# Optimization experiments

Hardware: AMD Instinct MI355X
Metric: run time of the kernel (lower is better)

The kernel has to match this reference:

```python
import jax, jax.numpy as jnp
import numpy as np

VOCAB = 100000
PAD_ID = 0
INTEREST_ID = 1
B, S, D = 16, 200, 128

def setup_inputs() -> dict:
    key = jax.random.key(0)
    ks = jax.random.split(key, 10)
    sc = 0.05
    return {
        "x": jax.random.normal(ks[0], (B, S, D), jnp.float32),
        "x_ids": jax.random.randint(ks[1], (B, S), 0, VOCAB),
        "Wq": jax.random.normal(ks[2], (D, D), jnp.float32) * sc,
        "bq": jax.random.normal(ks[3], (D,), jnp.float32) * sc,
        "Wk": jax.random.normal(ks[4], (D, D), jnp.float32) * sc,
        "bk": jax.random.normal(ks[5], (D,), jnp.float32) * sc,
        "Wv": jax.random.normal(ks[6], (D, 1), jnp.float32) * sc,
        "bv": jax.random.normal(ks[7], (1,), jnp.float32) * sc,
        "Wec": jax.random.normal(ks[8], (2 * D, VOCAB), jnp.float32) * sc,
        "bec": jax.random.normal(ks[9], (VOCAB,), jnp.float32) * sc,
    }

def reference(x, x_ids, Wq, bq, Wk, bk, Wv, bv, Wec, bec):
    # mask: valid (non-pad, non-interest) positions  (B,S)
    mask = (x_ids != PAD_ID) & (x_ids != INTEREST_ID)
    # additive attention pooling (explore_proj=True)
    q = jnp.einsum('bsd,de->bse', x, Wq) + bq            # (B,S,D)
    k = jnp.einsum('bd,de->be', x[:, 0, :], Wk) + bk      # (B,D), broadcast over S
    features = jnp.tanh(q + k[:, None, :])                # (B,S,D)
    scores = jnp.einsum('bsd,do->bso', features, Wv)[..., 0] + bv[0]  # (B,S)
    scores = jax.nn.softmax(scores, axis=-1)
    c_s = jnp.einsum('bsd,bs->bd', x, scores)             # (B,D)
    h_t = x[:, 0, :]                                      # (B,D)
    c_s = jnp.concatenate([h_t, c_s], axis=-1)            # (B,2D)
    p_explore = c_s @ Wec + bec                           # (B,V)
    # explore_mask: histogram of masked ids over vocab.
    # Equivalent to bmm(mask, one_hot(x_ids)) but O(B*S) scatter instead of O(B*S*V).
    explore_mask = jnp.zeros((x.shape[0], VOCAB), jnp.float32)
    batch_idx = jnp.arange(x.shape[0])[:, None]           # (B,1)
    explore_mask = explore_mask.at[batch_idx, x_ids].add(mask.astype(jnp.float32))
    p_explore = jnp.where(explore_mask > 0, -jnp.inf, p_explore)
    return jax.nn.softmax(p_explore, axis=-1)
```

## Files before the change

### kernel.cpp

```cpp
#include <hip/hip_runtime.h>
#include <cstdint>
#include <cstddef>
#include <math.h>

#define B 16
#define S 200
#define D 128
#define VOCAB 100000
#define V4 (VOCAB / 4)
#define SCH 8
#define VTILE 256
#define NVT ((VOCAB + VTILE - 1) / VTILE)

__global__ __launch_bounds__(128) void k_scores(
    const float* __restrict__ x,
    const float* __restrict__ Wq, const float* __restrict__ bq,
    const float* __restrict__ Wk, const float* __restrict__ bk,
    const float* __restrict__ Wv, const float* __restrict__ bv,
    float* __restrict__ scores)
{
  const int b  = blockIdx.x / (S / SCH);
  const int s0 = (blockIdx.x % (S / SCH)) * SCH;
  const int e  = threadIdx.x;

  __shared__ float lx[SCH][D];
  __shared__ float l0[D];
  __shared__ float sred[2][SCH];

  l0[e] = x[(size_t)b * S * D + e];
  #pragma unroll
  for (int i = 0; i < SCH; i++) lx[i][e] = x[((size_t)b * S + s0 + i) * D + e];
  __syncthreads();

  float q[SCH];
  const float bqe = bq[e];
  #pragma unroll
  for (int i = 0; i < SCH; i++) q[i] = bqe;
  float kk = bk[e];

  for (int d = 0; d < D; d++) {
    const float wq = Wq[d * D + e];
    const float wk = Wk[d * D + e];
    const float x0 = l0[d];
    kk += x0 * wk;
    #pragma unroll
    for (int i = 0; i < SCH; i++) q[i] += lx[i][d] * wq;
  }

  const float wv  = Wv[e];
  const float bv0 = bv[0];
  #pragma unroll
  for (int i = 0; i < SCH; i++) {
    float val = tanhf(q[i] + kk) * wv;
    #pragma unroll
    for (int off = 32; off > 0; off >>= 1) val += __shfl_down(val, off, 64);
    if ((e & 63) == 0) sred[e >> 6][i] = val;
  }
  __syncthreads();
  if (e < SCH) scores[b * S + s0 + e] = sred[0][e] + sred[1][e] + bv0;
}

__global__ __launch_bounds__(512) void k_csum(
    const float* __restrict__ x, const float* __restrict__ scores,
    float* __restrict__ cvec)
{
  const int b = blockIdx.x;
  const int t = threadIdx.x;
  __shared__ float pr[S];
  __shared__ float redm[9];
  __shared__ float reds[9];
  __shared__ float cpart[3][D];

  float v = (t < S) ? scores[b * S + t] : -INFINITY;
  float m = v;
  #pragma unroll
  for (int off = 32; off > 0; off >>= 1) m = fmaxf(m, __shfl_down(m, off, 64));
  if ((t & 63) == 0) redm[t >> 6] = m;
  __syncthreads();
  if (t == 0) {
    float mm = redm[0];
    #pragma unroll
    for (int i = 1; i < 8; i++) mm = fmaxf(mm, redm[i]);
    redm[8] = mm;
  }
  __syncthreads();
  const float mx = redm[8];

  float e = (t < S) ? expf(v - mx) : 0.f;
  float s = e;
  #pragma unroll
  for (int off = 32; off > 0; off >>= 1) s += __shfl_down(s, off, 64);
  if ((t & 63) == 0) reds[t >> 6] = s;
  __syncthreads();
  if (t == 0) {
    float ss = 0.f;
    #pragma unroll
    for (int i = 0; i < 8; i++) ss += reds[i];
    reds[8] = ss;
  }
  __syncthreads();
  const float inv = 1.0f / reds[8];
  if (t < S) pr[t] = e * inv;
  __syncthreads();

  const int d = t & 127;
  const int sq = t >> 7;
  float acc = 0.f;
  const float* xb = x + ((size_t)b * S + sq * 50) * D + d;
  #pragma unroll 5
  for (int s2 = 0; s2 < 50; s2++) acc += pr[sq * 50 + s2] * xb[s2 * D];
  if (sq) cpart[sq - 1][d] = acc;
  __syncthreads();
  if (sq == 0) {
    cvec[d * B + b]       = x[(size_t)b * S * D + d];
    cvec[(D + d) * B + b] = acc + cpart[0][d] + cpart[1][d] + cpart[2][d];
  }
}

__global__ __launch_bounds__(1024, 4) void k_gemv(
    const float* __restrict__ cvec, const float* __restrict__ Wec,
    const float* __restrict__ bec, const int* __restrict__ ids,
    float* __restrict__ out, float* __restrict__ partial)
{
  __shared__ float4 cbuf[16][4][64];
  __shared__ unsigned mbit[B * 8];

  const int t    = threadIdx.x;
  const int lane = t & 63;
  const int wv   = __builtin_amdgcn_readfirstlane(t >> 6);

  if (t < B * 8) mbit[t] = 0u;
  __syncthreads();

  const int vtile = blockIdx.x;
  const int vbase = vtile * VTILE;
  const int v4    = vtile * 64 + lane;
  const bool valid = (v4 < V4);
  const int v4c   = valid ? v4 : (V4 - 1);
  const int dbase = wv * 16;

  const float4* wp = (const float4*)Wec + v4c;

  const float4 creg = *(const float4*)&cvec[wv * 256 + lane * 4];

  for (int i = t; i < B * S; i += 1024) {
    const int id = ids[i];
    if (id > 1 && id >= vbase && id < vbase + VTILE) {
      const int lv = id - vbase;
      atomicOr(&mbit[(i / S) * 8 + (lv >> 5)], 1u << (lv & 31));
    }
  }

  float4 acc[16];
  #pragma unroll
  for (int i = 0; i < 16; i++) acc[i] = make_float4(0.f, 0.f, 0.f, 0.f);

#define RL(comp, sl) __int_as_float(__builtin_amdgcn_readlane(__float_as_int(comp), (sl)))

#define CONSUME(Wv, j)                                                     \
  { const float c0x = RL(creg.x, (j) * 4 + 0), c0y = RL(creg.y, (j) * 4 + 0); \
    const float c0z = RL(creg.z, (j) * 4 + 0), c0w = RL(creg.w, (j) * 4 + 0); \
    const float c1x = RL(creg.x, (j) * 4 + 1), c1y = RL(creg.y, (j) * 4 + 1); \
    const float c1z = RL(creg.z, (j) * 4 + 1), c1w = RL(creg.w, (j) * 4 + 1); \
    const float c2x = RL(creg.x, (j) * 4 + 2), c2y = RL(creg.y, (j) * 4 + 2); \
    const float c2z = RL(creg.z, (j) * 4 + 2), c2w = RL(creg.w, (j) * 4 + 2); \
    const float c3x = RL(creg.x, (j) * 4 + 3), c3y = RL(creg.y, (j) * 4 + 3); \
    const float c3z = RL(creg.z, (j) * 4 + 3), c3w = RL(creg.w, (j) * 4 + 3); \
    acc[0].x  = fmaf(Wv.x, c0x, acc[0].x);  acc[0].y  = fmaf(Wv.y, c0x, acc[0].y);  \
    acc[0].z  = fmaf(Wv.z, c0x, acc[0].z);  acc[0].w  = fmaf(Wv.w, c0x, acc[0].w);  \
    acc[1].x  = fmaf(Wv.x, c0y, acc[1].x);  acc[1].y  = fmaf(Wv.y, c0y, acc[1].y);  \
    acc[1].z  = fmaf(Wv.z, c0y, acc[1].z);  acc[1].w  = fmaf(Wv.w, c0y, acc[1].w);  \
    acc[2].x  = fmaf(Wv.x, c0z, acc[2].x);  acc[2].y  = fmaf(Wv.y, c0z, acc[2].y);  \
    acc[2].z  = fmaf(Wv.z, c0z, acc[2].z);  acc[2].w  = fmaf(Wv.w, c0z, acc[2].w);  \
    acc[3].x  = fmaf(Wv.x, c0w, acc[3].x);  acc[3].y  = fmaf(Wv.y, c0w, acc[3].y);  \
    acc[3].z  = fmaf(Wv.z, c0w, acc[3].z);  acc[3].w  = fmaf(Wv.w, c0w, acc[3].w);  \
    acc[4].x  = fmaf(Wv.x, c1x, acc[4].x);  acc[4].y  = fmaf(Wv.y, c1x, acc[4].y);  \
    acc[4].z  = fmaf(Wv.z, c1x, acc[4].z);  acc[4].w  = fmaf(Wv.w, c1x, acc[4].w);  \
    acc[5].x  = fmaf(Wv.x, c1y, acc[5].x);  acc[5].y  = fmaf(Wv.y, c1y, acc[5].y);  \
    acc[5].z  = fmaf(Wv.z, c1y, acc[5].z);  acc[5].w  = fmaf(Wv.w, c1y, acc[5].w);  \
    acc[6].x  = fmaf(Wv.x, c1z, acc[6].x);  acc[6].y  = fmaf(Wv.y, c1z, acc[6].y);  \
    acc[6].z  = fmaf(Wv.z, c1z, acc[6].z);  acc[6].w  = fmaf(Wv.w, c1z, acc[6].w);  \
    acc[7].x  = fmaf(Wv.x, c1w, acc[7].x);  acc[7].y  = fmaf(Wv.y, c1w, acc[7].y);  \
    acc[7].z  = fmaf(Wv.z, c1w, acc[7].z);  acc[7].w  = fmaf(Wv.w, c1w, acc[7].w);  \
    acc[8].x  = fmaf(Wv.x, c2x, acc[8].x);  acc[8].y  = fmaf(Wv.y, c2x, acc[8].y);  \
    acc[8].z  = fmaf(Wv.z, c2x, acc[8].z);  acc[8].w  = fmaf(Wv.w, c2x, acc[8].w);  \
    acc[9].x  = fmaf(Wv.x, c2y, acc[9].x);  acc[9].y  = fmaf(Wv.y, c2y, acc[9].y);  \
    acc[9].z  = fmaf(Wv.z, c2y, acc[9].z);  acc[9].w  = fmaf(Wv.w, c2y, acc[9].w);  \
    acc[10].x = fmaf(Wv.x, c2z, acc[10].x); acc[10].y = fmaf(Wv.y, c2z, acc[10].y); \
    acc[10].z = fmaf(Wv.z, c2z, acc[10].z); acc[10].w = fmaf(Wv.w, c2z, acc[10].w); \
    acc[11].x = fmaf(Wv.x, c2w, acc[11].x); acc[11].y = fmaf(Wv.y, c2w, acc[11].y); \
    acc[11].z = fmaf(Wv.z, c2w, acc[11].z); acc[11].w = fmaf(Wv.w, c2w, acc[11].w); \
    acc[12].x = fmaf(Wv.x, c3x, acc[12].x); acc[12].y = fmaf(Wv.y, c3x, acc[12].y); \
    acc[12].z = fmaf(Wv.z, c3x, acc[12].z); acc[12].w = fmaf(Wv.w, c3x, acc[12].w); \
    acc[13].x = fmaf(Wv.x, c3y, acc[13].x); acc[13].y = fmaf(Wv.y, c3y, acc[13].y); \
    acc[13].z = fmaf(Wv.z, c3y, acc[13].z); acc[13].w = fmaf(Wv.w, c3y, acc[13].w); \
    acc[14].x = fmaf(Wv.x, c3z, acc[14].x); acc[14].y = fmaf(Wv.y, c3z, acc[14].y); \
    acc[14].z = fmaf(Wv.z, c3z, acc[14].z); acc[14].w = fmaf(Wv.w, c3z, acc[14].w); \
    acc[15].x = fmaf(Wv.x, c3w, acc[15].x); acc[15].y = fmaf(Wv.y, c3w, acc[15].y); \
    acc[15].z = fmaf(Wv.z, c3w, acc[15].z); acc[15].w = fmaf(Wv.w, c3w, acc[15].w); }

  #pragma unroll
  for (int jj = 0; jj < 16; jj += 2) {
    const float4 w0 = wp[(size_t)(dbase + jj) * V4];
    const float4 w1 = wp[(size_t)(dbase + jj + 1) * V4];
    CONSUME(w0, jj)
    CONSUME(w1, jj + 1)
  }
#undef CONSUME
#undef RL

#define MASKED(bb, lv) ((mbit[(bb) * 8 + ((lv) >> 5)] >> ((lv) & 31)) & 1u)
  const float4 be4 = ((const float4*)bec)[v4c];
  const int lv0 = lane * 4;

  #pragma unroll
  for (int r = 0; r < 4; r++) {
    __syncthreads();
    #pragma unroll
    for (int i = 0; i < 4; i++) cbuf[wv][i][lane] = acc[r * 4 + i];
    __syncthreads();
    if (wv < 4) {
      const int bb = r * 4 + wv;
      float4 s = cbuf[0][wv][lane];
      #pragma unroll
      for (int sw = 1; sw < 16; sw++) {
        const float4 q = cbuf[sw][wv][lane];
        s.x += q.x; s.y += q.y; s.z += q.z; s.w += q.w;
      }
      float4 e = make_float4(0.f, 0.f, 0.f, 0.f);
      if (valid) {
        e.x = MASKED(bb, lv0 + 0) ? 0.f : __expf(s.x + be4.x);
        e.y = MASKED(bb, lv0 + 1) ? 0.f : __expf(s.y + be4.y);
        e.z = MASKED(bb, lv0 + 2) ? 0.f : __expf(s.z + be4.z);
        e.w = MASKED(bb, lv0 + 3) ? 0.f : __expf(s.w + be4.w);
        *(float4*)&out[(size_t)bb * VOCAB + (size_t)v4 * 4] = e;
      }
      float ps = e.x + e.y + e.z + e.w;
      #pragma unroll
      for (int off = 32; off > 0; off >>= 1) ps += __shfl_down(ps, off, 64);
      if (lane == 0) partial[vtile * 16 + bb] = ps;
    }
  }
#undef MASKED
}

__global__ __launch_bounds__(256) void k_norm(float* __restrict__ out,
                                              const float* __restrict__ partial)
{
  const int b  = blockIdx.y;
  const int t  = threadIdx.x;
  __shared__ float red[4];

  float s = 0.f;
  for (int j = t; j < NVT; j += 256) s += partial[j * 16 + b];
  #pragma unroll
  for (int off = 32; off > 0; off >>= 1) s += __shfl_down(s, off, 64);
  if ((t & 63) == 0) red[t >> 6] = s;
  __syncthreads();
  const float iv = 1.0f / (red[0] + red[1] + red[2] + red[3]);

  const int i4 = blockIdx.x * 256 + t;
  if (i4 < V4) {
    float4* p = (float4*)out + (size_t)b * V4 + i4;
    float4 q = *p;
    q.x *= iv; q.y *= iv; q.z *= iv; q.w *= iv;
    *p = q;
  }
}

extern "C" void kernel_launch(void* const* d_in, const int* in_sizes, int n_in,
                              void* d_out, int out_size, void* d_ws, size_t ws_size,
                              hipStream_t stream)
{
  const float* x   = (const float*)d_in[0];
  const int*   ids = (const int*)d_in[1];
  const float* Wq  = (const float*)d_in[2];
  const float* bq  = (const float*)d_in[3];
  const float* Wk  = (const float*)d_in[4];
  const float* bk  = (const float*)d_in[5];
  const float* Wv  = (const float*)d_in[6];
  const float* bv  = (const float*)d_in[7];
  const float* Wec = (const float*)d_in[8];
  const float* bec = (const float*)d_in[9];
  float* out = (float*)d_out;
  float* ws  = (float*)d_ws;

  float* scores  = ws;
  float* cvec    = ws + 3200;
  float* partial = ws + 7296;

  k_scores <<<dim3(B * (S / SCH)), dim3(128), 0, stream>>>(x, Wq, bq, Wk, bk, Wv, bv, scores);
  k_csum   <<<dim3(B),             dim3(512), 0, stream>>>(x, scores, cvec);
  k_gemv   <<<dim3(NVT),           dim3(1024), 0, stream>>>(cvec, Wec, bec, ids, out, partial);
  k_norm   <<<dim3((V4 + 255) / 256, B), dim3(256), 0, stream>>>(out, partial);
}
```

Baseline: 64.19 us.

## Stream Wec rows into LDS via async global_load_lds triple buffering

Replaces the direct float4 global loads of Wec in the GEMV kernel with asynchronous global-to-LDS copies (global_load_lds), staged through a three-deep per-wave ring buffer and drained with explicit vmcnt waits. The goal is to keep more weight loads in flight and overlap memory latency with the FMA/readlane work. The LDS arena grows to 96KB and is reused for the reduction buffer, which may cut occupancy (launch bounds request 4 blocks of 1024 threads). Out-of-range lanes in the tail tile reload lane offset 0.

```diff
diff --git a/kernel.cpp b/kernel.cpp
--- a/kernel.cpp
+++ b/kernel.cpp
@@ -11,6 +11,7 @@
 #define SCH 8
 #define VTILE 256
 #define NVT ((VOCAB + VTILE - 1) / VTILE)
+#define RCH 2
 
 __global__ __launch_bounds__(128) void k_scores(
     const float* __restrict__ x,
@@ -122,8 +123,9 @@
     const float* __restrict__ bec, const int* __restrict__ ids,
     float* __restrict__ out, float* __restrict__ partial)
 {
-  __shared__ float4 cbuf[16][4][64];
+  __shared__ __align__(16) char arena[98304];
   __shared__ unsigned mbit[B * 8];
+  float (*wbuf)[16][RCH][VTILE] = (float (*)[16][RCH][VTILE])arena;
 
   const int t    = threadIdx.x;
   const int lane = t & 63;
@@ -138,8 +140,7 @@
   const bool valid = (v4 < V4);
   const int v4c   = valid ? v4 : (V4 - 1);
   const int dbase = wv * 16;
-
-  const float4* wp = (const float4*)Wec + v4c;
+  const int laneoff = (vbase + lane * 4 + 3 < VOCAB) ? lane * 4 : 0;
 
   const float4 creg = *(const float4*)&cvec[wv * 256 + lane * 4];
 
@@ -155,9 +156,24 @@
   #pragma unroll
   for (int i = 0; i < 16; i++) acc[i] = make_float4(0.f, 0.f, 0.f, 0.f);
 
+#define STAGE(bufi, c)                                                      \
+  { _Pragma("unroll")                                                       \
+    for (int r = 0; r < RCH; r++) {                                         \
+      const int d = dbase + (c) * RCH + r;                                  \
+      const float* gp = Wec + (size_t)d * VOCAB + vbase + laneoff;          \
+      float* lp = &wbuf[bufi][wv][r][0];                                    \
+      __builtin_amdgcn_global_load_lds(                                     \
+          (const __attribute__((address_space(1))) void*)gp,                \
+          (__attribute__((address_space(3))) void*)lp, 16, 0, 0);           \
+    } }
+
+#define WAITC(n)                                                            \
+  { asm volatile("s_waitcnt vmcnt(" #n ")" ::: "memory");                   \
+    __builtin_amdgcn_sched_barrier(0); }
+
 #define RL(comp, sl) __int_as_float(__builtin_amdgcn_readlane(__float_as_int(comp), (sl)))
 
-#define CONSUME(Wv, j)                                                     \
+#define FMARL(Wr, j)                                                        \
   { const float c0x = RL(creg.x, (j) * 4 + 0), c0y = RL(creg.y, (j) * 4 + 0); \
     const float c0z = RL(creg.z, (j) * 4 + 0), c0w = RL(creg.w, (j) * 4 + 0); \
     const float c1x = RL(creg.x, (j) * 4 + 1), c1y = RL(creg.y, (j) * 4 + 1); \
@@ -166,48 +182,64 @@
     const float c2z = RL(creg.z, (j) * 4 + 2), c2w = RL(creg.w, (j) * 4 + 2); \
     const float c3x = RL(creg.x, (j) * 4 + 3), c3y = RL(creg.y, (j) * 4 + 3); \
     const float c3z = RL(creg.z, (j) * 4 + 3), c3w = RL(creg.w, (j) * 4 + 3); \
-    acc[0].x  = fmaf(Wv.x, c0x, acc[0].x);  acc[0].y  = fmaf(Wv.y, c0x, acc[0].y);  \
-    acc[0].z  = fmaf(Wv.z, c0x, acc[0].z);  acc[0].w  = fmaf(Wv.w, c0x, acc[0].w);  \
-    acc[1].x  = fmaf(Wv.x, c0y, acc[1].x);  acc[1].y  = fmaf(Wv.y, c0y, acc[1].y);  \
-    acc[1].z  = fmaf(Wv.z, c0y, acc[1].z);  acc[1].w  = fmaf(Wv.w, c0y, acc[1].w);  \
-    acc[2].x  = fmaf(Wv.x, c0z, acc[2].x);  acc[2].y  = fmaf(Wv.y, c0z, acc[2].y);  \
-    acc[2].z  = fmaf(Wv.z, c0z, acc[2].z);  acc[2].w  = fmaf(Wv.w, c0z, acc[2].w);  \
-    acc[3].x  = fmaf(Wv.x, c0w, acc[3].x);  acc[3].y  = fmaf(Wv.y, c0w, acc[3].y);  \
-    acc[3].z  = fmaf(Wv.z, c0w, acc[3].z);  acc[3].w  = fmaf(Wv.w, c0w, acc[3].w);  \
-    acc[4].x  = fmaf(Wv.x, c1x, acc[4].x);  acc[4].y  = fmaf(Wv.y, c1x, acc[4].y);  \
-    acc[4].z  = fmaf(Wv.z, c1x, acc[4].z);  acc[4].w  = fmaf(Wv.w, c1x, acc[4].w);  \
-    acc[5].x  = fmaf(Wv.x, c1y, acc[5].x);  acc[5].y  = fmaf(Wv.y, c1y, acc[5].y);  \
-    acc[5].z  = fmaf(Wv.z, c1y, acc[5].z);  acc[5].w  = fmaf(Wv.w, c1y, acc[5].w);  \
-    acc[6].x  = fmaf(Wv.x, c1z, acc[6].x);  acc[6].y  = fmaf(Wv.y, c1z, acc[6].y);  \
-    acc[6].z  = fmaf(Wv.z, c1z, acc[6].z);  acc[6].w  = fmaf(Wv.w, c1z, acc[6].w);  \
-    acc[7].x  = fmaf(Wv.x, c1w, acc[7].x);  acc[7].y  = fmaf(Wv.y, c1w, acc[7].y);  \
-    acc[7].z  = fmaf(Wv.z, c1w, acc[7].z);  acc[7].w  = fmaf(Wv.w, c1w, acc[7].w);  \
-    acc[8].x  = fmaf(Wv.x, c2x, acc[8].x);  acc[8].y  = fmaf(Wv.y, c2x, acc[8].y);  \
-    acc[8].z  = fmaf(Wv.z, c2x, acc[8].z);  acc[8].w  = fmaf(Wv.w, c2x, acc[8].w);  \
-    acc[9].x  = fmaf(Wv.x, c2y, acc[9].x);  acc[9].y  = fmaf(Wv.y, c2y, acc[9].y);  \
-    acc[9].z  = fmaf(Wv.z, c2y, acc[9].z);  acc[9].w  = fmaf(Wv.w, c2y, acc[9].w);  \
-    acc[10].x = fmaf(Wv.x, c2z, acc[10].x); acc[10].y = fmaf(Wv.y, c2z, acc[10].y); \
-    acc[10].z = fmaf(Wv.z, c2z, acc[10].z); acc[10].w = fmaf(Wv.w, c2z, acc[10].w); \
-    acc[11].x = fmaf(Wv.x, c2w, acc[11].x); acc[11].y = fmaf(Wv.y, c2w, acc[11].y); \
-    acc[11].z = fmaf(Wv.z, c2w, acc[11].z); acc[11].w = fmaf(Wv.w, c2w, acc[11].w); \
-    acc[12].x = fmaf(Wv.x, c3x, acc[12].x); acc[12].y = fmaf(Wv.y, c3x, acc[12].y); \
-    acc[12].z = fmaf(Wv.z, c3x, acc[12].z); acc[12].w = fmaf(Wv.w, c3x, acc[12].w); \
-    acc[13].x = fmaf(Wv.x, c3y, acc[13].x); acc[13].y = fmaf(Wv.y, c3y, acc[13].y); \
-    acc[13].z = fmaf(Wv.z, c3y, acc[13].z); acc[13].w = fmaf(Wv.w, c3y, acc[13].w); \
-    acc[14].x = fmaf(Wv.x, c3z, acc[14].x); acc[14].y = fmaf(Wv.y, c3z, acc[14].y); \
-    acc[14].z = fmaf(Wv.z, c3z, acc[14].z); acc[14].w = fmaf(Wv.w, c3z, acc[14].w); \
-    acc[15].x = fmaf(Wv.x, c3w, acc[15].x); acc[15].y = fmaf(Wv.y, c3w, acc[15].y); \
-    acc[15].z = fmaf(Wv.z, c3w, acc[15].z); acc[15].w = fmaf(Wv.w, c3w, acc[15].w); }
-
-  #pragma unroll
-  for (int jj = 0; jj < 16; jj += 2) {
-    const float4 w0 = wp[(size_t)(dbase + jj) * V4];
-    const float4 w1 = wp[(size_t)(dbase + jj + 1) * V4];
-    CONSUME(w0, jj)
-    CONSUME(w1, jj + 1)
-  }
+    acc[0].x  = fmaf(Wr.x, c0x, acc[0].x);  acc[0].y  = fmaf(Wr.y, c0x, acc[0].y);  \
+    acc[0].z  = fmaf(Wr.z, c0x, acc[0].z);  acc[0].w  = fmaf(Wr.w, c0x, acc[0].w);  \
+    acc[1].x  = fmaf(Wr.x, c0y, acc[1].x);  acc[1].y  = fmaf(Wr.y, c0y, acc[1].y);  \
+    acc[1].z  = fmaf(Wr.z, c0y, acc[1].z);  acc[1].w  = fmaf(Wr.w, c0y, acc[1].w);  \
+    acc[2].x  = fmaf(Wr.x, c0z, acc[2].x);  acc[2].y  = fmaf(Wr.y, c0z, acc[2].y);  \
+    acc[2].z  = fmaf(Wr.z, c0z, acc[2].z);  acc[2].w  = fmaf(Wr.w, c0z, acc[2].w);  \
+    acc[3].x  = fmaf(Wr.x, c0w, acc[3].x);  acc[3].y  = fmaf(Wr.y, c0w, acc[3].y);  \
+    acc[3].z  = fmaf(Wr.z, c0w, acc[3].z);  acc[3].w  = fmaf(Wr.w, c0w, acc[3].w);  \
+    acc[4].x  = fmaf(Wr.x, c1x, acc[4].x);  acc[4].y  = fmaf(Wr.y, c1x, acc[4].y);  \
+    acc[4].z  = fmaf(Wr.z, c1x, acc[4].z);  acc[4].w  = fmaf(Wr.w, c1x, acc[4].w);  \
+    acc[5].x  = fmaf(Wr.x, c1y, acc[5].x);  acc[5].y  = fmaf(Wr.y, c1y, acc[5].y);  \
+    acc[5].z  = fmaf(Wr.z, c1y, acc[5].z);  acc[5].w  = fmaf(Wr.w, c1y, acc[5].w);  \
+    acc[6].x  = fmaf(Wr.x, c1z, acc[6].x);  acc[6].y  = fmaf(Wr.y, c1z, acc[6].y);  \
+    acc[6].z  = fmaf(Wr.z, c1z, acc[6].z);  acc[6].w  = fmaf(Wr.w, c1z, acc[6].w);  \
+    acc[7].x  = fmaf(Wr.x, c1w, acc[7].x);  acc[7].y  = fmaf(Wr.y, c1w, acc[7].y);  \
+    acc[7].z  = fmaf(Wr.z, c1w, acc[7].z);  acc[7].w  = fmaf(Wr.w, c1w, acc[7].w);  \
+    acc[8].x  = fmaf(Wr.x, c2x, acc[8].x);  acc[8].y  = fmaf(Wr.y, c2x, acc[8].y);  \
+    acc[8].z  = fmaf(Wr.z, c2x, acc[8].z);  acc[8].w  = fmaf(Wr.w, c2x, acc[8].w);  \
+    acc[9].x  = fmaf(Wr.x, c2y, acc[9].x);  acc[9].y  = fmaf(Wr.y, c2y, acc[9].y);  \
+    acc[9].z  = fmaf(Wr.z, c2y, acc[9].z);  acc[9].w  = fmaf(Wr.w, c2y, acc[9].w);  \
+    acc[10].x = fmaf(Wr.x, c2z, acc[10].x); acc[10].y = fmaf(Wr.y, c2z, acc[10].y); \
+    acc[10].z = fmaf(Wr.z, c2z, acc[10].z); acc[10].w = fmaf(Wr.w, c2z, acc[10].w); \
+    acc[11].x = fmaf(Wr.x, c2w, acc[11].x); acc[11].y = fmaf(Wr.y, c2w, acc[11].y); \
+    acc[11].z = fmaf(Wr.z, c2w, acc[11].z); acc[11].w = fmaf(Wr.w, c2w, acc[11].w); \
+    acc[12].x = fmaf(Wr.x, c3x, acc[12].x); acc[12].y = fmaf(Wr.y, c3x, acc[12].y); \
+    acc[12].z = fmaf(Wr.z, c3x, acc[12].z); acc[12].w = fmaf(Wr.w, c3x, acc[12].w); \
+    acc[13].x = fmaf(Wr.x, c3y, acc[13].x); acc[13].y = fmaf(Wr.y, c3y, acc[13].y); \
+    acc[13].z = fmaf(Wr.z, c3y, acc[13].z); acc[13].w = fmaf(Wr.w, c3y, acc[13].w); \
+    acc[14].x = fmaf(Wr.x, c3z, acc[14].x); acc[14].y = fmaf(Wr.y, c3z, acc[14].y); \
+    acc[14].z = fmaf(Wr.z, c3z, acc[14].z); acc[14].w = fmaf(Wr.w, c3z, acc[14].w); \
+    acc[15].x = fmaf(Wr.x, c3w, acc[15].x); acc[15].y = fmaf(Wr.y, c3w, acc[15].y); \
+    acc[15].z = fmaf(Wr.z, c3w, acc[15].z); acc[15].w = fmaf(Wr.w, c3w, acc[15].w); }
+
+#define CONSUME(bufi, c)                                                    \
+  { const float4 w0 = *(const float4*)&wbuf[bufi][wv][0][lane * 4];         \
+    const float4 w1 = *(const float4*)&wbuf[bufi][wv][1][lane * 4];         \
+    FMARL(w0, (c) * 2 + 0)                                                  \
+    FMARL(w1, (c) * 2 + 1) }
+
+  STAGE(0, 0)
+  STAGE(1, 1)
+  STAGE(2, 2)  WAITC(4)  CONSUME(0, 0)
+  STAGE(0, 3)  WAITC(4)  CONSUME(1, 1)
+  STAGE(1, 4)  WAITC(4)  CONSUME(2, 2)
+  STAGE(2, 5)  WAITC(4)  CONSUME(0, 3)
+  STAGE(0, 6)  WAITC(4)  CONSUME(1, 4)
+  STAGE(1, 7)  WAITC(4)  CONSUME(2, 5)
+               WAITC(2)  CONSUME(0, 6)
+               WAITC(0)  CONSUME(1, 7)
+
 #undef CONSUME
+#undef FMARL
 #undef RL
+#undef WAITC
+#undef STAGE
+
+  __syncthreads();
+  float4 (*cbuf)[4][64] = (float4 (*)[4][64])arena;
 
 #define MASKED(bb, lv) ((mbit[(bb) * 8 + ((lv) >> 5)] >> ((lv) & 31)) & 1u)
   const float4 be4 = ((const float4*)bec)[v4c];
```

Result: slower. 71.47 us (+11.3%).
